# Kernel optimization log

Hardware: AMD Instinct MI355X
Metric: run time of the kernel (lower is better)

The kernel has to match this reference:

```python
import jax, jax.numpy as jnp
import numpy as np

N_NODES = 50000
N_EDGES = 800000
DIM = 128
LAYERS = 3


def setup_inputs() -> dict:
    key = jax.random.key(0)
    k1, k2, k3, k4 = jax.random.split(key, 4)
    x = jax.random.normal(k1, (N_NODES, DIM), dtype=jnp.float32)
    edge_index = jax.random.randint(k2, (2, N_EDGES), 0, N_NODES, dtype=jnp.int64)
    scale = 1.0 / np.sqrt(DIM)
    W_rel = jax.random.normal(k3, (LAYERS, DIM, DIM), dtype=jnp.float32) * scale
    W_root = jax.random.normal(k4, (LAYERS, DIM, DIM), dtype=jnp.float32) * scale
    b = jnp.zeros((LAYERS, DIM), dtype=jnp.float32)
    return {"x": x, "edge_index": edge_index, "W_rel": W_rel, "W_root": W_root, "b": b}


def graph_conv(x, src, dst, w_rel, w_root, bias):
    # message: gather source node features along each edge  [E, D]
    msg = x[src]
    # add-aggregation per destination node                  [N, D]
    agg = jax.ops.segment_sum(msg, dst, num_segments=N_NODES)
    # out_i = W_rel @ agg_i + W_root @ x_i + b
    return agg @ w_rel + x @ w_root + bias


def reference(x, edge_index, W_rel, W_root, b):
    src, dst = edge_index[0], edge_index[1]
    for l in range(LAYERS):
        x = graph_conv(x, src, dst, W_rel[l], W_root[l], b[l])
    return x
```

## Files before the change

### kernel.cpp

```cpp
#include <hip/hip_runtime.h>

#define N_NODES 50000
#define N_EDGES 800000
#define DIM     128
#define LAYERS  3

#define BSHIFT    7
#define N_BUCKETS 391
#define CHUNK     16384
#define N_CHUNKS  49

using short8 = __attribute__((ext_vector_type(8))) short;
using f32x4  = __attribute__((ext_vector_type(4))) float;

__device__ __forceinline__ unsigned short f2bf(float f) {
    unsigned int u = __builtin_bit_cast(unsigned int, f);
    unsigned int r = (u + 0x7fffu + ((u >> 16) & 1u)) >> 16;
    return (unsigned short)r;
}
__device__ __forceinline__ float bfl(unsigned int u) {
    return __builtin_bit_cast(float, u << 16);
}
__device__ __forceinline__ float bfh(unsigned int u) {
    return __builtin_bit_cast(float, u & 0xffff0000u);
}


__global__ __launch_bounds__(256) void convert_x(const float* __restrict__ x,
                                                 unsigned short* __restrict__ xb) {
    int t = blockIdx.x * 256 + threadIdx.x;
    size_t base = (size_t)t * 8;
    if (base >= (size_t)N_NODES * DIM) return;
    float4 v0 = *(const float4*)(x + base);
    float4 v1 = *(const float4*)(x + base + 4);
    uint4 o;
    o.x = ((unsigned)f2bf(v0.y) << 16) | f2bf(v0.x);
    o.y = ((unsigned)f2bf(v0.w) << 16) | f2bf(v0.z);
    o.z = ((unsigned)f2bf(v1.y) << 16) | f2bf(v1.x);
    o.w = ((unsigned)f2bf(v1.w) << 16) | f2bf(v1.z);
    *(uint4*)(xb + base) = o;
}

__global__ __launch_bounds__(256) void prep_w(const float* __restrict__ Wrel,
                                              const float* __restrict__ Wroot,
                                              unsigned short* __restrict__ Wt) {
    int t = blockIdx.x * 256 + threadIdx.x;
    if (t >= LAYERS * 2 * 128 * 32) return;
    int k4  = t & 31;
    int col = (t >> 5) & 127;
    int mat = (t >> 12) & 1;
    int l   = t >> 13;
    const float* W = (mat ? Wroot : Wrel) + (size_t)l * DIM * DIM;
    int k0 = k4 * 4;
    unsigned short b0 = f2bf(W[(size_t)(k0 + 0) * DIM + col]);
    unsigned short b1 = f2bf(W[(size_t)(k0 + 1) * DIM + col]);
    unsigned short b2 = f2bf(W[(size_t)(k0 + 2) * DIM + col]);
    unsigned short b3 = f2bf(W[(size_t)(k0 + 3) * DIM + col]);
    uint2 o;
    o.x = ((unsigned)b1 << 16) | b0;
    o.y = ((unsigned)b3 << 16) | b2;
    *(uint2*)(Wt + (size_t)l * 128 * 256 + (size_t)col * 256 + mat * 128 + k0) = o;
}


__global__ __launch_bounds__(1024) void bin_count(const int* __restrict__ dst,
                                                  int* __restrict__ bcnt) {
    __shared__ int hist[N_BUCKETS];
    int tid = threadIdx.x, chunk = blockIdx.x;
    for (int t = tid; t < N_BUCKETS; t += 1024) hist[t] = 0;
    __syncthreads();
    int base = chunk * CHUNK;
    for (int i = 0; i < CHUNK; i += 1024) {
        int e = base + i + tid;
        if (e < N_EDGES) atomicAdd(&hist[dst[e] >> BSHIFT], 1);
    }
    __syncthreads();
    for (int t = tid; t < N_BUCKETS; t += 1024)
        bcnt[t * N_CHUNKS + chunk] = hist[t];
}

__global__ __launch_bounds__(64) void bscan_a(const int* __restrict__ bcnt,
                                              int* __restrict__ boff,
                                              int* __restrict__ btot) {
    __shared__ int sh[64];
    int b = blockIdx.x, j = threadIdx.x;
    int v = (j < N_CHUNKS) ? bcnt[b * N_CHUNKS + j] : 0;
    sh[j] = v;
    __syncthreads();
    for (int off = 1; off < 64; off <<= 1) {
        int t = (j >= off) ? sh[j - off] : 0;
        __syncthreads();
        sh[j] += t;
        __syncthreads();
    }
    if (j < N_CHUNKS) boff[b * N_CHUNKS + j] = sh[j] - v;
    if (j == 63) btot[b] = sh[63];
}

__global__ __launch_bounds__(512) void bscan_b(const int* __restrict__ btot,
                                               int* __restrict__ bucket_start) {
    __shared__ int sh[512];
    int j = threadIdx.x;
    int v = (j < N_BUCKETS) ? btot[j] : 0;
    sh[j] = v;
    __syncthreads();
    for (int off = 1; off < 512; off <<= 1) {
        int t = (j >= off) ? sh[j - off] : 0;
        __syncthreads();
        sh[j] += t;
        __syncthreads();
    }
    if (j < N_BUCKETS) bucket_start[j] = sh[j] - v;
    if (j == N_BUCKETS - 1) bucket_start[N_BUCKETS] = sh[j];
}

__global__ __launch_bounds__(1024) void bin_scatter(const int* __restrict__ src,
                                                    const int* __restrict__ dst,
                                                    const int* __restrict__ bucket_start,
                                                    const int* __restrict__ boff,
                                                    unsigned int* __restrict__ pairs) {
    __shared__ int cur[N_BUCKETS];
    int tid = threadIdx.x, chunk = blockIdx.x;
    for (int t = tid; t < N_BUCKETS; t += 1024)
        cur[t] = bucket_start[t] + boff[t * N_CHUNKS + chunk];
    __syncthreads();
    int base = chunk * CHUNK;
    for (int i = 0; i < CHUNK; i += 1024) {
        int e = base + i + tid;
        if (e < N_EDGES) {
            int d = dst[e];
            int b = d >> BSHIFT;
            int p = atomicAdd(&cur[b], 1);
            pairs[p] = ((unsigned)(d & 127) << 16) | (unsigned)src[e];
        }
    }
}

__global__ __launch_bounds__(1024) void fill_lds(const unsigned int* __restrict__ pairs,
                                                 const int* __restrict__ bucket_start,
                                                 int* __restrict__ row_start,
                                                 unsigned short* __restrict__ srcs16) {
    __shared__ int hist[128];
    __shared__ int offs[128];
    __shared__ int cur[128];
    __shared__ unsigned short srt[4096];
    int b = blockIdx.x, tid = threadIdx.x;
    int s0 = bucket_start[b], s1 = bucket_start[b + 1];
    int cnt = s1 - s0;
    if (tid < 128) hist[tid] = 0;
    __syncthreads();
    for (int k = tid; k < cnt; k += 1024)
        atomicAdd(&hist[pairs[s0 + k] >> 16], 1);
    __syncthreads();
    if (tid < 128) offs[tid] = hist[tid];
    __syncthreads();
    for (int off = 1; off < 128; off <<= 1) {
        int t = 0;
        if (tid < 128 && tid >= off) t = offs[tid - off];
        __syncthreads();
        if (tid < 128) offs[tid] += t;
        __syncthreads();
    }
    if (tid < 128) {
        int excl = offs[tid] - hist[tid];
        cur[tid] = excl;
        int node = b * 128 + tid;
        if (node <= N_NODES) row_start[node] = s0 + excl;
    }
    __syncthreads();
    for (int k = tid; k < cnt; k += 1024) {
        unsigned int u = pairs[s0 + k];
        int p = atomicAdd(&cur[u >> 16], 1);
        srt[p] = (unsigned short)(u & 0xffffu);
    }
    __syncthreads();
    for (int k = tid; k < cnt; k += 1024)
        srcs16[s0 + k] = srt[k];
}


__device__ __forceinline__ void acc8(float* a, uint4 v) {
    a[0] += bfl(v.x); a[1] += bfh(v.x);
    a[2] += bfl(v.y); a[3] += bfh(v.y);
    a[4] += bfl(v.z); a[5] += bfh(v.z);
    a[6] += bfl(v.w); a[7] += bfh(v.w);
}

__global__ __launch_bounds__(256) void aggregate_bf16(const unsigned short* __restrict__ xb,
                                                      const int* __restrict__ row_start,
                                                      const unsigned short* __restrict__ srcs,
                                                      unsigned short* __restrict__ aggb) {
    int tid  = threadIdx.x;
    int L    = tid & 15;
    int node = blockIdx.x * 16 + (tid >> 4);
    if (node >= N_NODES) return;
    int beg = row_start[node];
    int end = row_start[node + 1];

    const uint4* xq = (const uint4*)xb;
    float a[8] = {0.f, 0.f, 0.f, 0.f, 0.f, 0.f, 0.f, 0.f};

    int j = beg;
    for (; j + 3 < end; j += 4) {
        uint4 v0 = xq[(size_t)srcs[j]     * 16 + L];
        uint4 v1 = xq[(size_t)srcs[j + 1] * 16 + L];
        uint4 v2 = xq[(size_t)srcs[j + 2] * 16 + L];
        uint4 v3 = xq[(size_t)srcs[j + 3] * 16 + L];
        acc8(a, v0); acc8(a, v1); acc8(a, v2); acc8(a, v3);
    }
    for (; j < end; ++j) {
        uint4 v = xq[(size_t)srcs[j] * 16 + L];
        acc8(a, v);
    }

    uint4 o;
    o.x = ((unsigned)f2bf(a[1]) << 16) | f2bf(a[0]);
    o.y = ((unsigned)f2bf(a[3]) << 16) | f2bf(a[2]);
    o.z = ((unsigned)f2bf(a[5]) << 16) | f2bf(a[4]);
    o.w = ((unsigned)f2bf(a[7]) << 16) | f2bf(a[6]);
    ((uint4*)aggb)[(size_t)node * 16 + L] = o;
}


__global__ __launch_bounds__(256) void gemm_bf16(const unsigned short* __restrict__ aggb,
                                                 const unsigned short* __restrict__ xb,
                                                 const unsigned short* __restrict__ Wt_l,
                                                 const float* __restrict__ bias,
                                                 unsigned short* __restrict__ outb,
                                                 float* __restrict__ outf) {
    __shared__ unsigned short Bs[128 * 256];

    int tid  = threadIdx.x;
    int lane = tid & 63;
    int w    = tid >> 6;

#pragma unroll
    for (int i = 0; i < 16; ++i) {
        int c   = tid + i * 256;
        int col = c >> 5;
        int q   = c & 31;
        uint4 v = ((const uint4*)Wt_l)[c];
        *(uint4*)&Bs[col * 256 + 8 * (q ^ (col & 7))] = v;
    }
    __syncthreads();

    int row0 = blockIdx.x * 128 + w * 32;

    f32x4 acc[2][8];
#pragma unroll
    for (int m = 0; m < 2; ++m)
#pragma unroll
        for (int n = 0; n < 8; ++n) acc[m][n] = (f32x4){0.f, 0.f, 0.f, 0.f};

    const short8 zero8 = {0, 0, 0, 0, 0, 0, 0, 0};

#pragma unroll
    for (int ch = 0; ch < 8; ++ch) {
        const unsigned short* Asrc = (ch < 4) ? aggb : xb;
        int k0 = (ch & 3) * 32 + (lane >> 4) * 8;

        short8 a[2];
#pragma unroll
        for (int m = 0; m < 2; ++m) {
            int r = row0 + m * 16 + (lane & 15);
            a[m] = (r < N_NODES) ? *(const short8*)(Asrc + (size_t)r * DIM + k0) : zero8;
        }

        int qbase = ch * 4 + (lane >> 4);
#pragma unroll
        for (int n = 0; n < 8; ++n) {
            int col = n * 16 + (lane & 15);
            short8 b = *(const short8*)&Bs[col * 256 + 8 * (qbase ^ (col & 7))];
            acc[0][n] = __builtin_amdgcn_mfma_f32_16x16x32_bf16(a[0], b, acc[0][n], 0, 0, 0);
            acc[1][n] = __builtin_amdgcn_mfma_f32_16x16x32_bf16(a[1], b, acc[1][n], 0, 0, 0);
        }
    }

#pragma unroll
    for (int n = 0; n < 8; ++n) {
        int col = n * 16 + (lane & 15);
        float bv = bias[col];
#pragma unroll
        for (int m = 0; m < 2; ++m) {
            int rb = row0 + m * 16 + (lane >> 4) * 4;
#pragma unroll
            for (int r = 0; r < 4; ++r) {
                int row = rb + r;
                if (row < N_NODES) {
                    float v = acc[m][n][r] + bv;
                    if (outf) outf[(size_t)row * DIM + col] = v;
                    else      outb[(size_t)row * DIM + col] = f2bf(v);
                }
            }
        }
    }
}


extern "C" void kernel_launch(void* const* d_in, const int* in_sizes, int n_in,
                              void* d_out, int out_size, void* d_ws, size_t ws_size,
                              hipStream_t stream) {
    const float* x0    = (const float*)d_in[0];
    const int*   ei    = (const int*)d_in[1];
    const float* Wrel  = (const float*)d_in[2];
    const float* Wroot = (const float*)d_in[3];
    const float* bvec  = (const float*)d_in[4];
    float* out = (float*)d_out;

    char* ws = (char*)d_ws;
    const size_t XB = (size_t)N_NODES * DIM * sizeof(unsigned short);
    unsigned short* xbA  = (unsigned short*)ws;
    unsigned short* xbB  = (unsigned short*)(ws + XB);
    unsigned short* aggb = (unsigned short*)(ws + 2 * XB);
    unsigned int* pairs  = (unsigned int*)(ws + 2 * XB);
    int* bcnt            = (int*)(ws + 2 * XB + 3200000);
    int* boff            = (int*)(ws + 2 * XB + 3276800);
    int* btot            = (int*)(ws + 2 * XB + 3353600);
    int* bucket_start    = (int*)(ws + 2 * XB + 3355648);
    unsigned short* Wt   = (unsigned short*)(ws + 3 * XB);
    unsigned short* srcs16 = (unsigned short*)(ws + 3 * XB + 196608);
    int* row_start       = (int*)(ws + 3 * XB + 196608 + 1600000);

    const int* src = ei;
    const int* dst = ei + N_EDGES;

    convert_x<<<(N_NODES * DIM / 8 + 255) / 256, 256, 0, stream>>>(x0, xbA);
    prep_w<<<(LAYERS * 2 * 128 * 32 + 255) / 256, 256, 0, stream>>>(Wrel, Wroot, Wt);

    bin_count<<<N_CHUNKS, 1024, 0, stream>>>(dst, bcnt);
    bscan_a<<<N_BUCKETS, 64, 0, stream>>>(bcnt, boff, btot);
    bscan_b<<<1, 512, 0, stream>>>(btot, bucket_start);
    bin_scatter<<<N_CHUNKS, 1024, 0, stream>>>(src, dst, bucket_start, boff, pairs);
    fill_lds<<<N_BUCKETS, 1024, 0, stream>>>(pairs, bucket_start, row_start, srcs16);

    unsigned short* xin = xbA;
    unsigned short* xouts[LAYERS] = {xbB, xbA, nullptr};
    for (int l = 0; l < LAYERS; ++l) {
        aggregate_bf16<<<(N_NODES + 15) / 16, 256, 0, stream>>>(xin, row_start, srcs16, aggb);
        gemm_bf16<<<(N_NODES + 127) / 128, 256, 0, stream>>>(
            aggb, xin, Wt + (size_t)l * 128 * 256, bvec + (size_t)l * DIM,
            xouts[l], (l == LAYERS - 1) ? out : nullptr);
        xin = xouts[l];
    }
}
```

Before: 255.7 us.

## Use smaller edge chunks, merge bucket scans, and unroll aggregation gather by eight

Cuts the edge chunk size so the binning kernels launch four times as many blocks and fill more compute units. The two bucket-scan kernels become one single-block kernel that walks chunks serially per bucket, using a transposed count layout, which saves one launch. The aggregation loop is unrolled to eight gathers in flight and the scalar tail loop is replaced by predicated loads. The single-block scan now does 196 serial steps per thread, which could offset the saved launch.

```diff
diff --git a/kernel.cpp b/kernel.cpp
--- a/kernel.cpp
+++ b/kernel.cpp
@@ -7,8 +7,8 @@
 
 #define BSHIFT    7
 #define N_BUCKETS 391
-#define CHUNK     16384
-#define N_CHUNKS  49
+#define CHUNK     4096
+#define N_CHUNKS  196
 
 using short8 = __attribute__((ext_vector_type(8))) short;
 using f32x4  = __attribute__((ext_vector_type(4))) float;
@@ -70,48 +70,39 @@
     for (int t = tid; t < N_BUCKETS; t += 1024) hist[t] = 0;
     __syncthreads();
     int base = chunk * CHUNK;
+#pragma unroll
     for (int i = 0; i < CHUNK; i += 1024) {
         int e = base + i + tid;
         if (e < N_EDGES) atomicAdd(&hist[dst[e] >> BSHIFT], 1);
     }
     __syncthreads();
     for (int t = tid; t < N_BUCKETS; t += 1024)
-        bcnt[t * N_CHUNKS + chunk] = hist[t];
-}
-
-__global__ __launch_bounds__(64) void bscan_a(const int* __restrict__ bcnt,
-                                              int* __restrict__ boff,
-                                              int* __restrict__ btot) {
-    __shared__ int sh[64];
-    int b = blockIdx.x, j = threadIdx.x;
-    int v = (j < N_CHUNKS) ? bcnt[b * N_CHUNKS + j] : 0;
-    sh[j] = v;
-    __syncthreads();
-    for (int off = 1; off < 64; off <<= 1) {
-        int t = (j >= off) ? sh[j - off] : 0;
+        bcnt[chunk * N_BUCKETS + t] = hist[t];
+}
+
+__global__ __launch_bounds__(512) void bscan(const int* __restrict__ bcnt,
+                                             int* __restrict__ boff,
+                                             int* __restrict__ bucket_start) {
+    __shared__ int sh[512];
+    int b = threadIdx.x;
+    int run = 0;
+    if (b < N_BUCKETS) {
+        for (int c = 0; c < N_CHUNKS; ++c) {
+            int v = bcnt[c * N_BUCKETS + b];
+            boff[c * N_BUCKETS + b] = run;
+            run += v;
+        }
+    }
+    sh[b] = (b < N_BUCKETS) ? run : 0;
+    __syncthreads();
+    for (int off = 1; off < 512; off <<= 1) {
+        int t = (b >= off) ? sh[b - off] : 0;
         __syncthreads();
-        sh[j] += t;
+        sh[b] += t;
         __syncthreads();
     }
-    if (j < N_CHUNKS) boff[b * N_CHUNKS + j] = sh[j] - v;
-    if (j == 63) btot[b] = sh[63];
-}
-
-__global__ __launch_bounds__(512) void bscan_b(const int* __restrict__ btot,
-                                               int* __restrict__ bucket_start) {
-    __shared__ int sh[512];
-    int j = threadIdx.x;
-    int v = (j < N_BUCKETS) ? btot[j] : 0;
-    sh[j] = v;
-    __syncthreads();
-    for (int off = 1; off < 512; off <<= 1) {
-        int t = (j >= off) ? sh[j - off] : 0;
-        __syncthreads();
-        sh[j] += t;
-        __syncthreads();
-    }
-    if (j < N_BUCKETS) bucket_start[j] = sh[j] - v;
-    if (j == N_BUCKETS - 1) bucket_start[N_BUCKETS] = sh[j];
+    if (b < N_BUCKETS) bucket_start[b] = sh[b] - run;
+    if (b == N_BUCKETS - 1) bucket_start[N_BUCKETS] = sh[b];
 }
 
 __global__ __launch_bounds__(1024) void bin_scatter(const int* __restrict__ src,
@@ -122,9 +113,10 @@
     __shared__ int cur[N_BUCKETS];
     int tid = threadIdx.x, chunk = blockIdx.x;
     for (int t = tid; t < N_BUCKETS; t += 1024)
-        cur[t] = bucket_start[t] + boff[t * N_CHUNKS + chunk];
+        cur[t] = bucket_start[t] + boff[chunk * N_BUCKETS + t];
     __syncthreads();
     int base = chunk * CHUNK;
+#pragma unroll
     for (int i = 0; i < CHUNK; i += 1024) {
         int e = base + i + tid;
         if (e < N_EDGES) {
@@ -194,23 +186,42 @@
     int L    = tid & 15;
     int node = blockIdx.x * 16 + (tid >> 4);
     if (node >= N_NODES) return;
-    int beg = row_start[node];
+    int j   = row_start[node];
     int end = row_start[node + 1];
 
     const uint4* xq = (const uint4*)xb;
     float a[8] = {0.f, 0.f, 0.f, 0.f, 0.f, 0.f, 0.f, 0.f};
 
-    int j = beg;
-    for (; j + 3 < end; j += 4) {
+    for (; j + 7 < end; j += 8) {
+        uint4 v0 = xq[(size_t)srcs[j]     * 16 + L];
+        uint4 v1 = xq[(size_t)srcs[j + 1] * 16 + L];
+        uint4 v2 = xq[(size_t)srcs[j + 2] * 16 + L];
+        uint4 v3 = xq[(size_t)srcs[j + 3] * 16 + L];
+        uint4 v4 = xq[(size_t)srcs[j + 4] * 16 + L];
+        uint4 v5 = xq[(size_t)srcs[j + 5] * 16 + L];
+        uint4 v6 = xq[(size_t)srcs[j + 6] * 16 + L];
+        uint4 v7 = xq[(size_t)srcs[j + 7] * 16 + L];
+        acc8(a, v0); acc8(a, v1); acc8(a, v2); acc8(a, v3);
+        acc8(a, v4); acc8(a, v5); acc8(a, v6); acc8(a, v7);
+    }
+    if (j + 3 < end) {
         uint4 v0 = xq[(size_t)srcs[j]     * 16 + L];
         uint4 v1 = xq[(size_t)srcs[j + 1] * 16 + L];
         uint4 v2 = xq[(size_t)srcs[j + 2] * 16 + L];
         uint4 v3 = xq[(size_t)srcs[j + 3] * 16 + L];
         acc8(a, v0); acc8(a, v1); acc8(a, v2); acc8(a, v3);
-    }
-    for (; j < end; ++j) {
-        uint4 v = xq[(size_t)srcs[j] * 16 + L];
-        acc8(a, v);
+        j += 4;
+    }
+    int rem = end - j;
+    if (rem > 0) {
+        int j1 = (rem > 1) ? j + 1 : j;
+        int j2 = (rem > 2) ? j + 2 : j;
+        uint4 v0 = xq[(size_t)srcs[j]  * 16 + L];
+        uint4 v1 = xq[(size_t)srcs[j1] * 16 + L];
+        uint4 v2 = xq[(size_t)srcs[j2] * 16 + L];
+        acc8(a, v0);
+        if (rem > 1) acc8(a, v1);
+        if (rem > 2) acc8(a, v2);
     }
 
     uint4 o;
@@ -314,9 +325,8 @@
     unsigned short* aggb = (unsigned short*)(ws + 2 * XB);
     unsigned int* pairs  = (unsigned int*)(ws + 2 * XB);
     int* bcnt            = (int*)(ws + 2 * XB + 3200000);
-    int* boff            = (int*)(ws + 2 * XB + 3276800);
-    int* btot            = (int*)(ws + 2 * XB + 3353600);
-    int* bucket_start    = (int*)(ws + 2 * XB + 3355648);
+    int* boff            = (int*)(ws + 2 * XB + 3506944);
+    int* bucket_start    = (int*)(ws + 2 * XB + 3813504);
     unsigned short* Wt   = (unsigned short*)(ws + 3 * XB);
     unsigned short* srcs16 = (unsigned short*)(ws + 3 * XB + 196608);
     int* row_start       = (int*)(ws + 3 * XB + 196608 + 1600000);
@@ -328,8 +338,7 @@
     prep_w<<<(LAYERS * 2 * 128 * 32 + 255) / 256, 256, 0, stream>>>(Wrel, Wroot, Wt);
 
     bin_count<<<N_CHUNKS, 1024, 0, stream>>>(dst, bcnt);
-    bscan_a<<<N_BUCKETS, 64, 0, stream>>>(bcnt, boff, btot);
-    bscan_b<<<1, 512, 0, stream>>>(btot, bucket_start);
+    bscan<<<1, 512, 0, stream>>>(bcnt, boff, bucket_start);
     bin_scatter<<<N_CHUNKS, 1024, 0, stream>>>(src, dst, bucket_start, boff, pairs);
     fill_lds<<<N_BUCKETS, 1024, 0, stream>>>(pairs, bucket_start, row_start, srcs16);
 
```

Measured after the change: 243.6 us. 4.7% less time.
